# Performance work log

Hardware: AMD Instinct MI355X
Metric: run time of the kernel (lower is better)

The kernel has to match this reference:

```python
import jax, jax.numpy as jnp
import numpy as np
import math

D = 768
H = 12
DFF = 3072
HD = D // H


def _layernorm(x, g, b, eps=1e-5):
    mu = jnp.mean(x, axis=-1, keepdims=True)
    var = jnp.var(x, axis=-1, keepdims=True)
    return (x - mu) * jax.lax.rsqrt(var + eps) * g + b


def setup_inputs() -> dict:
    key = jax.random.key(0)
    ks = jax.random.split(key, 12)
    B, S = 2, 4096
    s = 1.0 / math.sqrt(D)
    sf = 1.0 / math.sqrt(DFF)
    return {
        "x": jax.random.normal(ks[0], (B, S, D), jnp.float32),
        "attention_mask": jnp.ones((B, S), jnp.int32),
        "ln1_g": jnp.ones((D,), jnp.float32),
        "ln1_b": jnp.zeros((D,), jnp.float32),
        "ln2_g": jnp.ones((D,), jnp.float32),
        "ln2_b": jnp.zeros((D,), jnp.float32),
        "Wq": jax.random.normal(ks[1], (D, D), jnp.float32) * s,
        "bq": jnp.zeros((D,), jnp.float32),
        "Wk": jax.random.normal(ks[2], (D, D), jnp.float32) * s,
        "bk": jnp.zeros((D,), jnp.float32),
        "Wv": jax.random.normal(ks[3], (D, D), jnp.float32) * s,
        "bv": jnp.zeros((D,), jnp.float32),
        "Wo": jax.random.normal(ks[4], (D, D), jnp.float32) * s,
        "bo": jnp.zeros((D,), jnp.float32),
        "W1": jax.random.normal(ks[5], (D, DFF), jnp.float32) * s,
        "b1": jnp.zeros((DFF,), jnp.float32),
        "W2": jax.random.normal(ks[6], (DFF, D), jnp.float32) * sf,
        "b2": jnp.zeros((D,), jnp.float32),
    }


def _block(x, attention_mask, ln1_g, ln1_b, ln2_g, ln2_b,
           Wq, bq, Wk, bk, Wv, bv, Wo, bo, W1, b1, W2, b2):
    B, S, _ = x.shape
    h = _layernorm(x, ln1_g, ln1_b)
    q = (h @ Wq + bq).reshape(B, S, H, HD)
    k = (h @ Wk + bk).reshape(B, S, H, HD)
    v = (h @ Wv + bv).reshape(B, S, H, HD)
    # scores: [B, H, S, S]
    dots = jnp.einsum('bqhd,bkhd->bhqk', q, k) / math.sqrt(HD)
    causal = jnp.tril(jnp.ones((S, S), bool))  # True = keep
    keep = causal[None, None] & (attention_mask != 0)[:, None, None, :]
    dots = jnp.where(keep, dots, -jnp.inf)
    probs = jax.nn.softmax(dots, axis=-1)
    ctx = jnp.einsum('bhqk,bkhd->bqhd', probs, v).reshape(B, S, D)
    sa = ctx @ Wo + bo  # dropout = identity (eval)
    x = x + sa
    h2 = _layernorm(x, ln2_g, ln2_b)
    ff = jax.nn.relu(h2 @ W1 + b1) @ W2 + b2
    return x + ff


def reference(x, attention_mask, ln1_g, ln1_b, ln2_g, ln2_b,
              Wq, bq, Wk, bk, Wv, bv, Wo, bo, W1, b1, W2, b2):
    return _block(x, attention_mask, ln1_g, ln1_b, ln2_g, ln2_b,
                  Wq, bq, Wk, bk, Wv, bv, Wo, bo, W1, b1, W2, b2)
```

## Files before the change

### kernel.cpp

```cpp
#include <hip/hip_runtime.h>
#include <hip/hip_bf16.h>
#include <math.h>

#define S_LEN 4096
#define DMODEL 768
#define NHEAD 12
#define HDIM 64
#define DFF_ 3072
#define MROWS 8192

typedef __bf16 bf16;
typedef __bf16 bf16x4 __attribute__((ext_vector_type(4)));
typedef __bf16 bf16x8 __attribute__((ext_vector_type(8)));
typedef float f32x4 __attribute__((ext_vector_type(4)));
typedef short s16x4 __attribute__((ext_vector_type(4)));
typedef s16x4 frag4;

union F4 { float4 v; float f[4]; };
union U2 { bf16 h[2]; unsigned u; };
union P4 { unsigned u[2]; frag4 v; };

__device__ __forceinline__ void gld_lds16(void* lds, const void* g) {
    __builtin_amdgcn_global_load_lds(
        (const __attribute__((address_space(1))) unsigned int*)g,
        (__attribute__((address_space(3))) unsigned int*)lds, 16, 0, 0);
}

__device__ __forceinline__ f32x4 mfma16(frag4 a, frag4 b, f32x4 c) {
#if __has_builtin(__builtin_amdgcn_mfma_f32_16x16x16bf16_1k)
    return __builtin_amdgcn_mfma_f32_16x16x16bf16_1k(a, b, c, 0, 0, 0);
#else
    union { frag4 s; bf16x4 h; } ua, ub; ua.s = a; ub.s = b;
    bf16x8 a8 = {ua.h[0], ua.h[1], ua.h[2], ua.h[3],
                 (bf16)0.f, (bf16)0.f, (bf16)0.f, (bf16)0.f};
    bf16x8 b8 = {ub.h[0], ub.h[1], ub.h[2], ub.h[3],
                 (bf16)0.f, (bf16)0.f, (bf16)0.f, (bf16)0.f};
    return __builtin_amdgcn_mfma_f32_16x16x32_bf16(a8, b8, c, 0, 0, 0);
#endif
}

template<typename OUT>
__global__ __launch_bounds__(256) void ln_kernel(const float* __restrict__ x,
                                                 const float* __restrict__ g,
                                                 const float* __restrict__ bta,
                                                 OUT* __restrict__ out,
                                                 float* __restrict__ zb) {
    const int row = blockIdx.x;
    const int t = threadIdx.x;
    if (zb && row == 0 && t < 192)
        ((float4*)zb)[t] = make_float4(0.f, 0.f, 0.f, 0.f);
    const float* xr = x + (size_t)row * DMODEL;
    float v0 = xr[t], v1 = xr[t + 256], v2 = xr[t + 512];
    float s = v0 + v1 + v2;
    float ss = v0 * v0 + v1 * v1 + v2 * v2;
    for (int o = 32; o > 0; o >>= 1) {
        s += __shfl_down(s, o, 64);
        ss += __shfl_down(ss, o, 64);
    }
    __shared__ float sm[4], sm2[4];
    const int w = t >> 6, lane = t & 63;
    if (lane == 0) { sm[w] = s; sm2[w] = ss; }
    __syncthreads();
    s = sm[0] + sm[1] + sm[2] + sm[3];
    ss = sm2[0] + sm2[1] + sm2[2] + sm2[3];
    const float mu = s * (1.0f / DMODEL);
    const float var = ss * (1.0f / DMODEL) - mu * mu;
    const float rs = rsqrtf(var + 1e-5f);
    OUT* orow = out + (size_t)row * DMODEL;
    orow[t]       = (OUT)((v0 - mu) * rs * g[t]       + bta[t]);
    orow[t + 256] = (OUT)((v1 - mu) * rs * g[t + 256] + bta[t + 256]);
    orow[t + 512] = (OUT)((v2 - mu) * rs * g[t + 512] + bta[t + 512]);
}

__global__ __launch_bounds__(256) void wtrans_all_kernel(
    const float* __restrict__ Wq, const float* __restrict__ Wk,
    const float* __restrict__ Wv, const float* __restrict__ Wo,
    const float* __restrict__ W1, const float* __restrict__ W2,
    bf16* __restrict__ Wqt, bf16* __restrict__ Wkt, bf16* __restrict__ Wvt,
    bf16* __restrict__ Wot, bf16* __restrict__ W1t, bf16* __restrict__ W2t) {
    int t = blockIdx.x;
    const float* W; bf16* Wt; int K, N;
    if      (t < 144)  { W = Wq; Wt = Wqt; K = 768;  N = 768;  }
    else if (t < 288)  { W = Wk; Wt = Wkt; K = 768;  N = 768;  t -= 144; }
    else if (t < 432)  { W = Wv; Wt = Wvt; K = 768;  N = 768;  t -= 288; }
    else if (t < 576)  { W = Wo; Wt = Wot; K = 768;  N = 768;  t -= 432; }
    else if (t < 1152) { W = W1; Wt = W1t; K = 768;  N = 3072; t -= 576; }
    else               { W = W2; Wt = W2t; K = 3072; N = 768;  t -= 1152; }
    const int nx = N >> 6;
    const int n0 = (t % nx) * 64, k0 = (t / nx) * 64;

    __shared__ float tile[64][65];
    const int tid = threadIdx.x;
    const int lr = tid >> 4, lc = (tid & 15) << 2;
#pragma unroll
    for (int i = 0; i < 4; ++i) {
        const int r = lr + i * 16;
        F4 w; w.v = *(const float4*)&W[(size_t)(k0 + r) * N + n0 + lc];
#pragma unroll
        for (int j = 0; j < 4; ++j) tile[r][lc + j] = w.f[j];
    }
    __syncthreads();
#pragma unroll
    for (int i = 0; i < 4; ++i) {
        const int n = lr + i * 16;
        bf16x4 o;
#pragma unroll
        for (int j = 0; j < 4; ++j) o[j] = (bf16)tile[lc + j][n];
        *(bf16x4*)&Wt[(size_t)(n0 + n) * K + k0 + lc] = o;
    }
}

__global__ __launch_bounds__(256) void vtrans_kernel(const bf16* __restrict__ vb,
                                                     bf16* __restrict__ vbt) {
    const int kt = blockIdx.x, h = blockIdx.y, b = blockIdx.z;
    __shared__ bf16 tile[64][65];
    const int t = threadIdx.x;
    const int kl = t >> 2, ds = (t & 3) * 16;
    const bf16* src = vb + (size_t)(b * S_LEN + kt * 64 + kl) * DMODEL + h * HDIM + ds;
    *(bf16x8*)&tile[kl][ds]     = *(const bf16x8*)src;
    *(bf16x8*)&tile[kl][ds + 8] = *(const bf16x8*)(src + 8);
    __syncthreads();
    const int d = t >> 2;
    bf16* drow = vbt + (size_t)((b * NHEAD + h) * HDIM + d) * S_LEN + kt * 64;
#pragma unroll
    for (int c = 0; c < 2; ++c) {
        const int k0 = (t & 3) * 16 + c * 8;
        bf16x8 o;
#pragma unroll
        for (int j = 0; j < 8; ++j) o[j] = tile[k0 + j][d];
        *(bf16x8*)(drow + k0) = o;
    }
}

template<int MT, bool RELU, bool RES, bool OUT_BF16>
__global__ __launch_bounds__(256) void mgemm_kernel(
    const bf16* __restrict__ A,
    const bf16* __restrict__ Wt0, const float* __restrict__ bias0, void* __restrict__ C0,
    const bf16* __restrict__ Wt1, const float* __restrict__ bias1, void* __restrict__ C1,
    const bf16* __restrict__ Wt2, const float* __restrict__ bias2, void* __restrict__ C2,
    const float* __restrict__ R, int M, int N, int K, int Kloop,
    int koff0, int koff1, int koff2,
    float sc0, float sc1, float sc2) {
    const bf16* Wt = Wt0; const float* bias = bias0; void* C = C0; float sc = sc0; int koff = koff0;
    if (blockIdx.z == 1) { Wt = Wt1; bias = bias1; C = C1; sc = sc1; koff = koff1; }
    if (blockIdx.z == 2) { Wt = Wt2; bias = bias2; C = C2; sc = sc2; koff = koff2; }

    const int gx = gridDim.x;
    const int nwg = gx * gridDim.y;
    const int chunk = nwg >> 3;
    int lid = blockIdx.y * gx + blockIdx.x;
    lid = (lid & 7) * chunk + (lid >> 3);
    const int row0 = (lid / gx) * MT, col0 = (lid % gx) * 128;

    constexpr int NI = (MT == 128) ? 4 : 2;
    __shared__ bf16 As[2][MT * 32];
    __shared__ bf16 Bs[2][128 * 32];

    const int tid = threadIdx.x;
    const int wave = tid >> 6, lane = tid & 63;
    const int wr = (MT == 128) ? (wave >> 1) * 64 : 0;
    const int wc = (MT == 128) ? (wave & 1) * 64 : wave * 32;
    const int mrow = lane & 15, kq = (lane >> 4) * 8;

    const int st_row = (lane >> 2);
    const int st_off = (lane & 3) * 16;

    f32x4 acc[4][NI] = {};

    const char* Ab = (const char*)(A + (size_t)row0 * K + koff);
    const char* Bb = (const char*)(Wt + (size_t)col0 * K + koff);
    const size_t strideA = (size_t)K * 2;

    for (int k0 = 0; k0 < Kloop; k0 += 64) {
#pragma unroll
        for (int s = 0; s < 2; ++s) {
            const int kk = k0 + s * 32;
            if (MT == 128) {
#pragma unroll
                for (int issue = 0; issue < 2; ++issue) {
                    const int r = wave * 32 + issue * 16 + st_row;
                    gld_lds16((char*)As[s] + (wave * 32 + issue * 16) * 64,
                              Ab + (size_t)r * strideA + kk * 2 + st_off);
                }
            } else {
                const int r = wave * 16 + st_row;
                gld_lds16((char*)As[s] + (wave * 16) * 64,
                          Ab + (size_t)r * strideA + kk * 2 + st_off);
            }
#pragma unroll
            for (int issue = 0; issue < 2; ++issue) {
                const int r = wave * 32 + issue * 16 + st_row;
                gld_lds16((char*)Bs[s] + (wave * 32 + issue * 16) * 64,
                          Bb + (size_t)r * strideA + kk * 2 + st_off);
            }
        }
        __syncthreads();
#pragma unroll
        for (int s = 0; s < 2; ++s) {
            bf16x8 af[4], bfr[NI];
#pragma unroll
            for (int mi = 0; mi < 4; ++mi)
                af[mi] = *(const bf16x8*)&As[s][(wr + mi * 16 + mrow) * 32 + kq];
#pragma unroll
            for (int ni = 0; ni < NI; ++ni)
                bfr[ni] = *(const bf16x8*)&Bs[s][(wc + ni * 16 + mrow) * 32 + kq];
#pragma unroll
            for (int mi = 0; mi < 4; ++mi)
#pragma unroll
                for (int ni = 0; ni < NI; ++ni)
                    acc[mi][ni] = __builtin_amdgcn_mfma_f32_16x16x32_bf16(
                        bfr[ni], af[mi], acc[mi][ni], 0, 0, 0);
        }
        __syncthreads();
    }

    const int quad = lane >> 4;
#pragma unroll
    for (int ni = 0; ni < NI; ++ni) {
        const int col = col0 + wc + ni * 16 + quad * 4;
        F4 bv4; bv4.v = *(const float4*)&bias[col];
#pragma unroll
        for (int mi = 0; mi < 4; ++mi) {
            const int row = row0 + wr + mi * 16 + mrow;
            F4 o;
#pragma unroll
            for (int r = 0; r < 4; ++r) o.f[r] = acc[mi][ni][r] + bv4.f[r];
            if (RES) {
                F4 rr; rr.v = *(const float4*)&R[(size_t)row * N + col];
#pragma unroll
                for (int r = 0; r < 4; ++r) o.f[r] += rr.f[r];
            }
#pragma unroll
            for (int r = 0; r < 4; ++r) {
                o.f[r] *= sc;
                if (RELU) o.f[r] = fmaxf(o.f[r], 0.0f);
            }
            if (OUT_BF16) {
                bf16x4 ob;
#pragma unroll
                for (int r = 0; r < 4; ++r) ob[r] = (bf16)o.f[r];
                *(bf16x4*)&((bf16*)C)[(size_t)row * N + col] = ob;
            } else {
                *(float4*)&((float*)C)[(size_t)row * N + col] = o.v;
            }
        }
    }
}

__global__ __launch_bounds__(256) void mattn_kernel(
    const bf16* __restrict__ Q, const bf16* __restrict__ K,
    const bf16* __restrict__ Vt, const int* __restrict__ amask,
    bf16* __restrict__ O) {
    const int bx = blockIdx.x, h = blockIdx.y, b = blockIdx.z;

    __shared__ bf16 Ks[2][4096];
    __shared__ bf16 Vs[2][4096];
    __shared__ bf16 Os[64][68];
    __shared__ float mk[2][64];
    __shared__ int flagv[2];

    const int tid = threadIdx.x;
    const int wave = tid >> 6, lane = tid & 63;
    const int l = lane & 15, quad = lane >> 4;
    const float NEG_INF = -__builtin_huge_valf();

    const int g1 = 256 + tid;
    const int rw0 = tid >> 3, pc0 = tid & 7;
    const int rw1 = g1 >> 3,  pc1 = g1 & 7;
    const int koff0 = rw0 * DMODEL + ((pc0 ^ (rw0 & 7)) << 3);
    const int koff1 = rw1 * DMODEL + ((pc1 ^ (rw1 & 7)) << 3);
    const int voff0 = rw0 * S_LEN + ((pc0 ^ (rw0 & 7)) << 3);
    const int voff1 = rw1 * S_LEN + ((pc1 ^ (rw1 & 7)) << 3);

    const bf16* Kbase = K + (size_t)b * S_LEN * DMODEL + h * HDIM;
    const bf16* Vtb = Vt + (size_t)((b * NHEAD + h) * HDIM) * S_LEN;

    const int sw = (l & 7) << 4;
    const int krd0 = l * 128 + ((quad << 4) ^ sw);
    const int krd1 = l * 128 + (((4 + quad) << 4) ^ sw);

    P4 onesu; onesu.u[0] = 0x3F803F80u; onesu.u[1] = 0x3F803F80u;
    const frag4 onesA = onesu.v;

#pragma unroll 1
    for (int pass = 0; pass < 2; ++pass) {
        const int qt = pass ? bx : (63 - bx);

        const bf16* Qb = Q + (size_t)(b * S_LEN + qt * 64 + wave * 16 + l) * DMODEL + h * HDIM;
        const bf16x8 qf0 = *(const bf16x8*)(Qb + quad * 8);
        const bf16x8 qf1 = *(const bf16x8*)(Qb + 32 + quad * 8);

        float m_run = NEG_INF;
        f32x4 acc[4] = {};
        f32x4 acc_l = {};

        {
            char* kd = (char*)Ks[0] + wave * 1024;
            char* vd = (char*)Vs[0] + wave * 1024;
            gld_lds16(kd,        Kbase + koff0);
            gld_lds16(kd + 4096, Kbase + koff1);
            gld_lds16(vd,        Vtb + voff0);
            gld_lds16(vd + 4096, Vtb + voff1);
            if (wave == 0) {
                int mv0 = amask[b * S_LEN + lane];
                mk[0][lane] = mv0 ? 0.0f : NEG_INF;
                unsigned long long bal = __ballot(mv0 != 0);
                if (lane == 0) flagv[0] = (bal == ~0ULL);
            }
        }
        __syncthreads();
        int buf = 0;
        int mv = 1;

        for (int kt = 0; kt <= qt; ++kt) {
            const bool more = (kt < qt);
            if (more) {
                const bf16* kg = Kbase + (size_t)(kt + 1) * 64 * DMODEL;
                const bf16* vg = Vtb + (kt + 1) * 64;
                const int nb = buf ^ 1;
                char* kd = (char*)Ks[nb] + wave * 1024;
                char* vd = (char*)Vs[nb] + wave * 1024;
                gld_lds16(kd,        kg + koff0);
                gld_lds16(kd + 4096, kg + koff1);
                gld_lds16(vd,        vg + voff0);
                gld_lds16(vd + 4096, vg + voff1);
                if (wave == 0) mv = amask[b * S_LEN + (kt + 1) * 64 + lane];
            }

            const int allv = flagv[buf];
            const char* Ksb = (const char*)Ks[buf];
            const char* Vsb = (const char*)Vs[buf];
            f32x4 sreg[4] = {};
            __builtin_amdgcn_s_setprio(1);
#pragma unroll
            for (int mi = 0; mi < 4; ++mi) {
                bf16x8 kf0 = *(const bf16x8*)(Ksb + mi * 2048 + krd0);
                bf16x8 kf1 = *(const bf16x8*)(Ksb + mi * 2048 + krd1);
                sreg[mi] = __builtin_amdgcn_mfma_f32_16x16x32_bf16(kf0, qf0, sreg[mi], 0, 0, 0);
                sreg[mi] = __builtin_amdgcn_mfma_f32_16x16x32_bf16(kf1, qf1, sreg[mi], 0, 0, 0);
            }
            __builtin_amdgcn_s_setprio(0);
            if (!allv) {
#pragma unroll
                for (int mi = 0; mi < 4; ++mi) {
                    F4 m4; m4.v = *(const float4*)&mk[buf][mi * 16 + quad * 4];
#pragma unroll
                    for (int r = 0; r < 4; ++r) sreg[mi][r] += m4.f[r];
                }
            }
            if (kt == qt) {
#pragma unroll
                for (int mi = 0; mi < 4; ++mi)
#pragma unroll
                    for (int r = 0; r < 4; ++r)
                        if (mi * 16 + quad * 4 + r > wave * 16 + l)
                            sreg[mi][r] = NEG_INF;
            }

            float mloc = sreg[0][0];
#pragma unroll
            for (int mi = 0; mi < 4; ++mi)
#pragma unroll
                for (int r = 0; r < 4; ++r) mloc = fmaxf(mloc, sreg[mi][r]);
            mloc = fmaxf(mloc, __shfl_xor(mloc, 16, 64));
            mloc = fmaxf(mloc, __shfl_xor(mloc, 32, 64));
            if (__any(mloc > m_run + 8.0f)) {
                const float mn = fmaxf(m_run, mloc);
                const float alpha = __builtin_amdgcn_exp2f(m_run - mn);
                m_run = mn;
#pragma unroll
                for (int di = 0; di < 4; ++di)
#pragma unroll
                    for (int r = 0; r < 4; ++r) acc[di][r] *= alpha;
#pragma unroll
                for (int r = 0; r < 4; ++r) acc_l[r] *= alpha;
            }
#pragma unroll
            for (int mi = 0; mi < 4; ++mi)
#pragma unroll
                for (int r = 0; r < 4; ++r)
                    sreg[mi][r] = __builtin_amdgcn_exp2f(sreg[mi][r] - m_run);

            unsigned pk[4][2];
#pragma unroll
            for (int mi = 0; mi < 4; ++mi) {
                U2 w0; w0.h[0] = (bf16)sreg[mi][0]; w0.h[1] = (bf16)sreg[mi][1];
                U2 w1; w1.h[0] = (bf16)sreg[mi][2]; w1.h[1] = (bf16)sreg[mi][3];
                pk[mi][0] = w0.u; pk[mi][1] = w1.u;
            }

            __builtin_amdgcn_s_setprio(1);
#pragma unroll
            for (int mi = 0; mi < 4; ++mi) {
                P4 pb; pb.u[0] = pk[mi][0]; pb.u[1] = pk[mi][1];
                const int vb_mi = (((mi << 5) | (quad << 3)) ^ sw);
#pragma unroll
                for (int di = 0; di < 4; ++di) {
                    frag4 va = *(const frag4*)(Vsb + di * 2048 + l * 128 + vb_mi);
                    acc[di] = mfma16(va, pb.v, acc[di]);
                }
                acc_l = mfma16(onesA, pb.v, acc_l);
            }
            __builtin_amdgcn_s_setprio(0);

            if (more && wave == 0) {
                const int nb = buf ^ 1;
                mk[nb][lane] = mv ? 0.0f : NEG_INF;
                unsigned long long bal = __ballot(mv != 0);
                if (lane == 0) flagv[nb] = (bal == ~0ULL);
            }
            __syncthreads();
            buf ^= 1;
        }

        const float l_fin = __shfl(acc_l[0], l, 64);
        const float rinv = 1.0f / l_fin;
#pragma unroll
        for (int mi = 0; mi < 4; ++mi) {
            U2 w0; w0.h[0] = (bf16)(acc[mi][0] * rinv); w0.h[1] = (bf16)(acc[mi][1] * rinv);
            U2 w1; w1.h[0] = (bf16)(acc[mi][2] * rinv); w1.h[1] = (bf16)(acc[mi][3] * rinv);
            *(unsigned*)&Os[wave * 16 + l][mi * 16 + quad * 4]     = w0.u;
            *(unsigned*)&Os[wave * 16 + l][mi * 16 + quad * 4 + 2] = w1.u;
        }
        __syncthreads();
        {
            const int orow = tid >> 2, oseg = (tid & 3) * 16;
            bf16* Og = O + (size_t)(b * S_LEN + qt * 64 + orow) * DMODEL + h * HDIM + oseg;
            *(bf16x8*)Og       = *(const bf16x8*)&Os[orow][oseg];
            *(bf16x8*)(Og + 8) = *(const bf16x8*)&Os[orow][oseg + 8];
        }
        __syncthreads();
    }
}

extern "C" void kernel_launch(void* const* d_in, const int* in_sizes, int n_in,
                              void* d_out, int out_size, void* d_ws, size_t ws_size,
                              hipStream_t stream) {
    const float* x     = (const float*)d_in[0];
    const int*   amask = (const int*)  d_in[1];
    const float* ln1_g = (const float*)d_in[2];
    const float* ln1_b = (const float*)d_in[3];
    const float* ln2_g = (const float*)d_in[4];
    const float* ln2_b = (const float*)d_in[5];
    const float* Wq = (const float*)d_in[6];  const float* bq = (const float*)d_in[7];
    const float* Wk = (const float*)d_in[8];  const float* bk = (const float*)d_in[9];
    const float* Wv = (const float*)d_in[10]; const float* bv = (const float*)d_in[11];
    const float* Wo = (const float*)d_in[12]; const float* bo = (const float*)d_in[13];
    const float* W1 = (const float*)d_in[14]; const float* b1 = (const float*)d_in[15];
    const float* W2 = (const float*)d_in[16]; const float* b2 = (const float*)d_in[17];
    float* out = (float*)d_out;

    char* ws = (char*)d_ws;
    const size_t WSML = (size_t)DMODEL * DMODEL * 2;
    const size_t WBIG = (size_t)DMODEL * DFF_ * 2;
    bf16* Wqt = (bf16*)(ws + 0 * WSML);
    bf16* Wkt = (bf16*)(ws + 1 * WSML);
    bf16* Wvt = (bf16*)(ws + 2 * WSML);
    bf16* Wot = (bf16*)(ws + 3 * WSML);
    bf16* W1t = (bf16*)(ws + 4 * WSML);
    bf16* W2t = (bf16*)(ws + 4 * WSML + WBIG);
    char* act = ws + 4 * WSML + 2 * WBIG;

    const size_t HB = (size_t)MROWS * DMODEL * 2;
    const size_t FB = (size_t)MROWS * DMODEL * 4;
    bf16*  h    = (bf16*)(act);
    bf16*  qb   = (bf16*)(act + HB);
    bf16*  kb   = (bf16*)(act + 2 * HB);
    bf16*  vb   = (bf16*)(act + 3 * HB);
    bf16*  ctx  = h;
    float* x1   = (float*)(act + 4 * HB);
    bf16*  f    = (bf16*)(act + 4 * HB + FB);
    bf16*  h2   = h;
    bf16*  vbt  = f;

    const float SCL = 0.125f * 1.44269504089f;

    wtrans_all_kernel<<<1728, 256, 0, stream>>>(Wq, Wk, Wv, Wo, W1, W2,
                                                Wqt, Wkt, Wvt, Wot, W1t, W2t);

    ln_kernel<bf16><<<MROWS, 256, 0, stream>>>(x, ln1_g, ln1_b, h, nullptr);
    mgemm_kernel<128, false, false, true><<<dim3(DMODEL / 128, MROWS / 128, 3), 256, 0, stream>>>(
        h, Wqt, bq, qb, Wkt, bk, kb, Wvt, bv, vb, nullptr,
        MROWS, DMODEL, DMODEL, DMODEL, 0, 0, 0, SCL, 1.0f, 1.0f);
    vtrans_kernel<<<dim3(S_LEN / 64, NHEAD, 2), 256, 0, stream>>>(vb, vbt);
    mattn_kernel<<<dim3(32, NHEAD, 2), 256, 0, stream>>>(qb, kb, vbt, amask, ctx);
    mgemm_kernel<64, false, true, false><<<dim3(DMODEL / 128, MROWS / 64, 1), 256, 0, stream>>>(
        ctx, Wot, bo, x1, Wot, bo, x1, Wot, bo, x1, x,
        MROWS, DMODEL, DMODEL, DMODEL, 0, 0, 0, 1.0f, 1.0f, 1.0f);
    ln_kernel<bf16><<<MROWS, 256, 0, stream>>>(x1, ln2_g, ln2_b, h2, nullptr);
    mgemm_kernel<128, true, false, true><<<dim3(DFF_ / 128, MROWS / 128, 1), 256, 0, stream>>>(
        h2, W1t, b1, f, W1t, b1, f, W1t, b1, f, nullptr,
        MROWS, DFF_, DMODEL, DMODEL, 0, 0, 0, 1.0f, 1.0f, 1.0f);
    mgemm_kernel<64, false, true, false><<<dim3(DMODEL / 128, MROWS / 64, 1), 256, 0, stream>>>(
        f, W2t, b2, out, W2t, b2, out, W2t, b2, out, x1,
        MROWS, DMODEL, DFF_, DFF_, 0, 0, 0, 1.0f, 1.0f, 1.0f);
}
```

Baseline: 450.4 us.

## Switch GEMM to 32x32x16 MFMA with swizzled LDS and merge weight prep with LN1

The GEMM kernel moves from 16x16x32 to 32x32x16 bf16 MFMA tiles. Each wave now holds 2xNI 16-wide accumulators, and LDS reads use an XOR-swizzled layout to avoid bank conflicts, with the global-to-LDS store offsets swizzled to match. The weight transpose/convert kernel and the first layernorm are fused into a single launch to remove one kernel boundary. The risk is that the swizzle mapping and the new epilogue layout must match the MFMA output ordering exactly.

```diff
diff --git a/kernel.cpp b/kernel.cpp
--- a/kernel.cpp
+++ b/kernel.cpp
@@ -13,6 +13,7 @@
 typedef __bf16 bf16x4 __attribute__((ext_vector_type(4)));
 typedef __bf16 bf16x8 __attribute__((ext_vector_type(8)));
 typedef float f32x4 __attribute__((ext_vector_type(4)));
+typedef float f32x16 __attribute__((ext_vector_type(16)));
 typedef short s16x4 __attribute__((ext_vector_type(4)));
 typedef s16x4 frag4;
 
@@ -39,6 +40,70 @@
 #endif
 }
 
+__global__ __launch_bounds__(256) void pre_kernel(
+    const float* __restrict__ Wq, const float* __restrict__ Wk,
+    const float* __restrict__ Wv, const float* __restrict__ Wo,
+    const float* __restrict__ W1, const float* __restrict__ W2,
+    bf16* __restrict__ Wqt, bf16* __restrict__ Wkt, bf16* __restrict__ Wvt,
+    bf16* __restrict__ Wot, bf16* __restrict__ W1t, bf16* __restrict__ W2t,
+    const float* __restrict__ x, const float* __restrict__ g,
+    const float* __restrict__ bta, bf16* __restrict__ hout) {
+    const int tid = threadIdx.x;
+    if (blockIdx.x < 1728) {
+        int t = blockIdx.x;
+        const float* W; bf16* Wt; int K, N;
+        if      (t < 144)  { W = Wq; Wt = Wqt; K = 768;  N = 768;  }
+        else if (t < 288)  { W = Wk; Wt = Wkt; K = 768;  N = 768;  t -= 144; }
+        else if (t < 432)  { W = Wv; Wt = Wvt; K = 768;  N = 768;  t -= 288; }
+        else if (t < 576)  { W = Wo; Wt = Wot; K = 768;  N = 768;  t -= 432; }
+        else if (t < 1152) { W = W1; Wt = W1t; K = 768;  N = 3072; t -= 576; }
+        else               { W = W2; Wt = W2t; K = 3072; N = 768;  t -= 1152; }
+        const int nx = N >> 6;
+        const int n0 = (t % nx) * 64, k0 = (t / nx) * 64;
+        __shared__ float tile[64][65];
+        const int lr = tid >> 4, lc = (tid & 15) << 2;
+#pragma unroll
+        for (int i = 0; i < 4; ++i) {
+            const int r = lr + i * 16;
+            F4 w; w.v = *(const float4*)&W[(size_t)(k0 + r) * N + n0 + lc];
+#pragma unroll
+            for (int j = 0; j < 4; ++j) tile[r][lc + j] = w.f[j];
+        }
+        __syncthreads();
+#pragma unroll
+        for (int i = 0; i < 4; ++i) {
+            const int n = lr + i * 16;
+            bf16x4 o;
+#pragma unroll
+            for (int j = 0; j < 4; ++j) o[j] = (bf16)tile[lc + j][n];
+            *(bf16x4*)&Wt[(size_t)(n0 + n) * K + k0 + lc] = o;
+        }
+    } else {
+        const int row = blockIdx.x - 1728;
+        const float* xr = x + (size_t)row * DMODEL;
+        float v0 = xr[tid], v1 = xr[tid + 256], v2 = xr[tid + 512];
+        float s = v0 + v1 + v2;
+        float ss = v0 * v0 + v1 * v1 + v2 * v2;
+        for (int o = 32; o > 0; o >>= 1) {
+            s += __shfl_down(s, o, 64);
+            ss += __shfl_down(ss, o, 64);
+        }
+        __shared__ float sm[4], sm2[4];
+        const int w = tid >> 6, lane = tid & 63;
+        if (lane == 0) { sm[w] = s; sm2[w] = ss; }
+        __syncthreads();
+        s = sm[0] + sm[1] + sm[2] + sm[3];
+        ss = sm2[0] + sm2[1] + sm2[2] + sm2[3];
+        const float mu = s * (1.0f / DMODEL);
+        const float var = ss * (1.0f / DMODEL) - mu * mu;
+        const float rs = rsqrtf(var + 1e-5f);
+        bf16* orow = hout + (size_t)row * DMODEL;
+        orow[tid]       = (bf16)((v0 - mu) * rs * g[tid]       + bta[tid]);
+        orow[tid + 256] = (bf16)((v1 - mu) * rs * g[tid + 256] + bta[tid + 256]);
+        orow[tid + 512] = (bf16)((v2 - mu) * rs * g[tid + 512] + bta[tid + 512]);
+    }
+}
+
 template<typename OUT>
 __global__ __launch_bounds__(256) void ln_kernel(const float* __restrict__ x,
                                                  const float* __restrict__ g,
@@ -47,8 +112,6 @@
                                                  float* __restrict__ zb) {
     const int row = blockIdx.x;
     const int t = threadIdx.x;
-    if (zb && row == 0 && t < 192)
-        ((float4*)zb)[t] = make_float4(0.f, 0.f, 0.f, 0.f);
     const float* xr = x + (size_t)row * DMODEL;
     float v0 = xr[t], v1 = xr[t + 256], v2 = xr[t + 512];
     float s = v0 + v1 + v2;
@@ -72,44 +135,6 @@
     orow[t + 512] = (OUT)((v2 - mu) * rs * g[t + 512] + bta[t + 512]);
 }
 
-__global__ __launch_bounds__(256) void wtrans_all_kernel(
-    const float* __restrict__ Wq, const float* __restrict__ Wk,
-    const float* __restrict__ Wv, const float* __restrict__ Wo,
-    const float* __restrict__ W1, const float* __restrict__ W2,
-    bf16* __restrict__ Wqt, bf16* __restrict__ Wkt, bf16* __restrict__ Wvt,
-    bf16* __restrict__ Wot, bf16* __restrict__ W1t, bf16* __restrict__ W2t) {
-    int t = blockIdx.x;
-    const float* W; bf16* Wt; int K, N;
-    if      (t < 144)  { W = Wq; Wt = Wqt; K = 768;  N = 768;  }
-    else if (t < 288)  { W = Wk; Wt = Wkt; K = 768;  N = 768;  t -= 144; }
-    else if (t < 432)  { W = Wv; Wt = Wvt; K = 768;  N = 768;  t -= 288; }
-    else if (t < 576)  { W = Wo; Wt = Wot; K = 768;  N = 768;  t -= 432; }
-    else if (t < 1152) { W = W1; Wt = W1t; K = 768;  N = 3072; t -= 576; }
-    else               { W = W2; Wt = W2t; K = 3072; N = 768;  t -= 1152; }
-    const int nx = N >> 6;
-    const int n0 = (t % nx) * 64, k0 = (t / nx) * 64;
-
-    __shared__ float tile[64][65];
-    const int tid = threadIdx.x;
-    const int lr = tid >> 4, lc = (tid & 15) << 2;
-#pragma unroll
-    for (int i = 0; i < 4; ++i) {
-        const int r = lr + i * 16;
-        F4 w; w.v = *(const float4*)&W[(size_t)(k0 + r) * N + n0 + lc];
-#pragma unroll
-        for (int j = 0; j < 4; ++j) tile[r][lc + j] = w.f[j];
-    }
-    __syncthreads();
-#pragma unroll
-    for (int i = 0; i < 4; ++i) {
-        const int n = lr + i * 16;
-        bf16x4 o;
-#pragma unroll
-        for (int j = 0; j < 4; ++j) o[j] = (bf16)tile[lc + j][n];
-        *(bf16x4*)&Wt[(size_t)(n0 + n) * K + k0 + lc] = o;
-    }
-}
-
 __global__ __launch_bounds__(256) void vtrans_kernel(const bf16* __restrict__ vb,
                                                      bf16* __restrict__ vbt) {
     const int kt = blockIdx.x, h = blockIdx.y, b = blockIdx.z;
@@ -152,7 +177,7 @@
     lid = (lid & 7) * chunk + (lid >> 3);
     const int row0 = (lid / gx) * MT, col0 = (lid % gx) * 128;
 
-    constexpr int NI = (MT == 128) ? 4 : 2;
+    constexpr int NI = (MT == 128) ? 2 : 1;
     __shared__ bf16 As[2][MT * 32];
     __shared__ bf16 Bs[2][128 * 32];
 
@@ -160,12 +185,13 @@
     const int wave = tid >> 6, lane = tid & 63;
     const int wr = (MT == 128) ? (wave >> 1) * 64 : 0;
     const int wc = (MT == 128) ? (wave & 1) * 64 : wave * 32;
-    const int mrow = lane & 15, kq = (lane >> 4) * 8;
+    const int r5 = lane & 31, khalf = lane >> 5;
+    const int rsw = (r5 >> 1) & 3;
 
     const int st_row = (lane >> 2);
-    const int st_off = (lane & 3) * 16;
-
-    f32x4 acc[4][NI] = {};
+    const int st_off = (((lane & 3) ^ ((lane >> 3) & 3)) << 4);
+
+    f32x16 acc[2][NI] = {};
 
     const char* Ab = (const char*)(A + (size_t)row0 * K + koff);
     const char* Bb = (const char*)(Wt + (size_t)col0 * K + koff);
@@ -197,51 +223,61 @@
         __syncthreads();
 #pragma unroll
         for (int s = 0; s < 2; ++s) {
-            bf16x8 af[4], bfr[NI];
-#pragma unroll
-            for (int mi = 0; mi < 4; ++mi)
-                af[mi] = *(const bf16x8*)&As[s][(wr + mi * 16 + mrow) * 32 + kq];
+            bf16x8 af[2][2], bfr[NI][2];
+#pragma unroll
+            for (int mi = 0; mi < 2; ++mi)
+#pragma unroll
+                for (int kc = 0; kc < 2; ++kc)
+                    af[mi][kc] = *(const bf16x8*)((const char*)As[s] +
+                        (wr + mi * 32 + r5) * 64 + (((kc * 2 + khalf) ^ rsw) << 4));
 #pragma unroll
             for (int ni = 0; ni < NI; ++ni)
-                bfr[ni] = *(const bf16x8*)&Bs[s][(wc + ni * 16 + mrow) * 32 + kq];
-#pragma unroll
-            for (int mi = 0; mi < 4; ++mi)
+#pragma unroll
+                for (int kc = 0; kc < 2; ++kc)
+                    bfr[ni][kc] = *(const bf16x8*)((const char*)Bs[s] +
+                        (wc + ni * 32 + r5) * 64 + (((kc * 2 + khalf) ^ rsw) << 4));
+#pragma unroll
+            for (int mi = 0; mi < 2; ++mi)
 #pragma unroll
                 for (int ni = 0; ni < NI; ++ni)
-                    acc[mi][ni] = __builtin_amdgcn_mfma_f32_16x16x32_bf16(
-                        bfr[ni], af[mi], acc[mi][ni], 0, 0, 0);
+#pragma unroll
+                    for (int kc = 0; kc < 2; ++kc)
+                        acc[mi][ni] = __builtin_amdgcn_mfma_f32_32x32x16_bf16(
+                            bfr[ni][kc], af[mi][kc], acc[mi][ni], 0, 0, 0);
         }
         __syncthreads();
     }
 
-    const int quad = lane >> 4;
 #pragma unroll
     for (int ni = 0; ni < NI; ++ni) {
-        const int col = col0 + wc + ni * 16 + quad * 4;
-        F4 bv4; bv4.v = *(const float4*)&bias[col];
-#pragma unroll
-        for (int mi = 0; mi < 4; ++mi) {
-            const int row = row0 + wr + mi * 16 + mrow;
-            F4 o;
-#pragma unroll
-            for (int r = 0; r < 4; ++r) o.f[r] = acc[mi][ni][r] + bv4.f[r];
-            if (RES) {
-                F4 rr; rr.v = *(const float4*)&R[(size_t)row * N + col];
-#pragma unroll
-                for (int r = 0; r < 4; ++r) o.f[r] += rr.f[r];
-            }
-#pragma unroll
-            for (int r = 0; r < 4; ++r) {
-                o.f[r] *= sc;
-                if (RELU) o.f[r] = fmaxf(o.f[r], 0.0f);
-            }
-            if (OUT_BF16) {
-                bf16x4 ob;
-#pragma unroll
-                for (int r = 0; r < 4; ++r) ob[r] = (bf16)o.f[r];
-                *(bf16x4*)&((bf16*)C)[(size_t)row * N + col] = ob;
-            } else {
-                *(float4*)&((float*)C)[(size_t)row * N + col] = o.v;
+#pragma unroll
+        for (int g = 0; g < 4; ++g) {
+            const int col = col0 + wc + ni * 32 + g * 8 + khalf * 4;
+            F4 bv4; bv4.v = *(const float4*)&bias[col];
+#pragma unroll
+            for (int mi = 0; mi < 2; ++mi) {
+                const int row = row0 + wr + mi * 32 + r5;
+                F4 o;
+#pragma unroll
+                for (int r = 0; r < 4; ++r) o.f[r] = acc[mi][ni][g * 4 + r] + bv4.f[r];
+                if (RES) {
+                    F4 rr; rr.v = *(const float4*)&R[(size_t)row * N + col];
+#pragma unroll
+                    for (int r = 0; r < 4; ++r) o.f[r] += rr.f[r];
+                }
+#pragma unroll
+                for (int r = 0; r < 4; ++r) {
+                    o.f[r] *= sc;
+                    if (RELU) o.f[r] = fmaxf(o.f[r], 0.0f);
+                }
+                if (OUT_BF16) {
+                    bf16x4 ob;
+#pragma unroll
+                    for (int r = 0; r < 4; ++r) ob[r] = (bf16)o.f[r];
+                    *(bf16x4*)&((bf16*)C)[(size_t)row * N + col] = ob;
+                } else {
+                    *(float4*)&((float*)C)[(size_t)row * N + col] = o.v;
+                }
             }
         }
     }
@@ -475,10 +511,9 @@
 
     const float SCL = 0.125f * 1.44269504089f;
 
-    wtrans_all_kernel<<<1728, 256, 0, stream>>>(Wq, Wk, Wv, Wo, W1, W2,
-                                                Wqt, Wkt, Wvt, Wot, W1t, W2t);
-
-    ln_kernel<bf16><<<MROWS, 256, 0, stream>>>(x, ln1_g, ln1_b, h, nullptr);
+    pre_kernel<<<1728 + MROWS, 256, 0, stream>>>(Wq, Wk, Wv, Wo, W1, W2,
+                                                 Wqt, Wkt, Wvt, Wot, W1t, W2t,
+                                                 x, ln1_g, ln1_b, h);
     mgemm_kernel<128, false, false, true><<<dim3(DMODEL / 128, MROWS / 128, 3), 256, 0, stream>>>(
         h, Wqt, bq, qb, Wkt, bk, kb, Wvt, bv, vb, nullptr,
         MROWS, DMODEL, DMODEL, DMODEL, 0, 0, 0, SCL, 1.0f, 1.0f);
```

Result: slower. 469.4 us (+4.2%).
